# Kernel tuning notes

Hardware: AMD Instinct MI355X
Metric: run time of the kernel (lower is better)

Reference implementation:

```python
import jax, jax.numpy as jnp
import numpy as np

N = 1_000_000
D = 128            # node feature dim
G = 25_000         # number of graphs (num_segments, static)
STEPS = 8


def setup_inputs() -> dict:
    key = jax.random.key(0)
    k1, k2, k3 = jax.random.split(key, 3)
    node_feature = jax.random.normal(k1, (N, D), dtype=jnp.float32)
    graph_indicator = jnp.sort(jax.random.randint(k2, (N,), 0, G, dtype=jnp.int32))
    # glorot-ish small init for recurrent kernel (carry_dim=2D -> 4*D gates)
    recurrent_kernel = jax.random.normal(k3, (2 * D, 4 * D), dtype=jnp.float32) * 0.05
    bias = jnp.zeros((4 * D,), dtype=jnp.float32)
    return {
        "node_feature": node_feature,
        "graph_indicator": graph_indicator,
        "recurrent_kernel": recurrent_kernel,
        "bias": bias,
    }


def _segment_softmax(score, seg_ids, num_segments):
    # numerically-stable per-segment softmax over a flat score vector [N]
    smax = jax.ops.segment_max(score, seg_ids, num_segments=num_segments)
    e = jnp.exp(score - smax[seg_ids])
    denom = jax.ops.segment_sum(e, seg_ids, num_segments=num_segments)
    return e / denom[seg_ids]


def reference(node_feature, graph_indicator, recurrent_kernel, bias):
    d = node_feature.shape[-1]
    memory_state = jnp.zeros((G, d), dtype=node_feature.dtype)
    carry_state = jnp.zeros((G, d), dtype=node_feature.dtype)
    carry_state_evolved = None
    for _ in range(STEPS):
        # attention score per node: <node_feature, carry of its graph>
        carry_exp = carry_state[graph_indicator]                  # [N, d]
        score = jnp.sum(node_feature * carry_exp, axis=1)         # [N]
        attn = _segment_softmax(score, graph_indicator, G)        # [N]
        readout = jax.ops.segment_sum(attn[:, None] * node_feature,
                                      graph_indicator, num_segments=G)  # [G, d]
        carry_state_evolved = jnp.concatenate([carry_state, readout], axis=1)  # [G, 2d]
        # NoInputLSTMCell
        z = carry_state_evolved @ recurrent_kernel + bias          # [G, 4d]
        u, f, c, o = jnp.split(z, 4, axis=1)
        memory_state = jax.nn.sigmoid(f) * memory_state + jax.nn.sigmoid(u) * jnp.tanh(c)
        carry_state = jax.nn.sigmoid(o) * jnp.tanh(memory_state)
    return carry_state_evolved
```

## Files before the change

### kernel.cpp

```cpp
#include <hip/hip_runtime.h>
#include <stdint.h>

#define DD  128
#define G2D 256
#define G4D 512

typedef float  f32x4  __attribute__((ext_vector_type(4)));
typedef short  s16x8  __attribute__((ext_vector_type(8)));
typedef __bf16 bf16x8 __attribute__((ext_vector_type(8)));

__device__ __forceinline__ short f2bf(float f) {
  unsigned u = __builtin_bit_cast(unsigned, f);
  u += 0x7FFFu + ((u >> 16) & 1u);
  return (short)(u >> 16);
}
__device__ __forceinline__ float bf2f(short s) {
  unsigned u = ((unsigned)(unsigned short)s) << 16;
  return __builtin_bit_cast(float, u);
}
__device__ __forceinline__ float sigmoidf_(float x) {
  return 1.f / (1.f + __expf(-x));
}
__device__ __forceinline__ float tanhf_(float x) {
  x = fminf(fmaxf(x, -15.f), 15.f);
  float e = __expf(2.f * x);
  return (e - 1.f) / (e + 1.f);
}

__global__ void seg_kernel(const int* __restrict__ ind, int* __restrict__ seg,
                           int N, int G) {
  int g = blockIdx.x * blockDim.x + threadIdx.x;
  if (g > G) return;
  int lo = 0, hi = N;
  while (lo < hi) {
    int mid = (lo + hi) >> 1;
    if (ind[mid] < g) lo = mid + 1; else hi = mid;
  }
  seg[g] = lo;
}

__global__ void nfconv_kernel(const float* __restrict__ nf,
                              short* __restrict__ nfb) {
  size_t idx = (size_t)blockIdx.x * blockDim.x + threadIdx.x;
  const f32x4* src = (const f32x4*)nf + idx * 2;
  f32x4 a = src[0], b = src[1];
  s16x8 o;
  o[0] = f2bf(a.x); o[1] = f2bf(a.y); o[2] = f2bf(a.z); o[3] = f2bf(a.w);
  o[4] = f2bf(b.x); o[5] = f2bf(b.y); o[6] = f2bf(b.z); o[7] = f2bf(b.w);
  ((s16x8*)nfb)[idx] = o;
}

__global__ void wconv_kernel(const float* __restrict__ W, short* __restrict__ WT) {
  int idx = blockIdx.x * blockDim.x + threadIdx.x;
  int n = idx & (G4D - 1);
  int k = idx >> 9;
  WT[(size_t)n * G2D + k] = f2bf(W[(size_t)k * G4D + n]);
}

__global__ void __launch_bounds__(256) passa_kernel(
    const short* __restrict__ nfb, float* __restrict__ ce,
    const int* __restrict__ seg, int G) {
  int wid = (blockIdx.x * blockDim.x + threadIdx.x) >> 6;
  if (wid >= G) return;
  int lane = threadIdx.x & 63;
  int gq = lane >> 4;
  int sl = lane & 15;
  int s0 = seg[wid], s1 = seg[wid + 1];
  int n  = s1 - s0;
  float* cerow = ce + (size_t)wid * G2D;
  if (n == 0) {
    if (gq == 0) {
      f32x4 z = {0.f, 0.f, 0.f, 0.f};
      *(f32x4*)(cerow + DD + sl * 8)     = z;
      *(f32x4*)(cerow + DD + sl * 8 + 4) = z;
    }
    return;
  }
  f32x4 c0 = *(const f32x4*)(cerow + sl * 8);
  f32x4 c1 = *(const f32x4*)(cerow + sl * 8 + 4);
  float m = -1e30f, l = 0.f;
  float acc[8];
  #pragma unroll
  for (int k = 0; k < 8; k++) acc[k] = 0.f;
  const short* base = nfb + (size_t)s0 * DD + sl * 8;

  auto body = [&](int j) {
    s16x8 xr = *(const s16x8*)(base + (size_t)j * DD);
    float xf[8];
    #pragma unroll
    for (int k = 0; k < 8; k++) xf[k] = bf2f(xr[k]);
    float s = xf[0]*c0.x + xf[1]*c0.y + xf[2]*c0.z + xf[3]*c0.w
            + xf[4]*c1.x + xf[5]*c1.y + xf[6]*c1.z + xf[7]*c1.w;
    #pragma unroll
    for (int off = 1; off < 16; off <<= 1) s += __shfl_xor(s, off, 64);
    float nm = fmaxf(m, s);
    float sc = __expf(m - nm);
    float p  = __expf(s - nm);
    l = l * sc + p;
    #pragma unroll
    for (int k = 0; k < 8; k++) acc[k] = acc[k] * sc + p * xf[k];
    m = nm;
  };

  int nfull = n >> 2;
  #pragma unroll 2
  for (int i = 0; i < nfull; i++) body(i * 4 + gq);
  int rem = n & 3;
  if (gq < rem) body(nfull * 4 + gq);

  #pragma unroll
  for (int w = 16; w <= 32; w <<= 1) {
    float m2 = __shfl_xor(m, w, 64);
    float l2 = __shfl_xor(l, w, 64);
    float M  = fmaxf(m, m2);
    float e1 = __expf(m - M);
    float e2 = __expf(m2 - M);
    l = l * e1 + l2 * e2;
    #pragma unroll
    for (int k = 0; k < 8; k++) {
      float a2 = __shfl_xor(acc[k], w, 64);
      acc[k] = acc[k] * e1 + a2 * e2;
    }
    m = M;
  }
  if (gq == 0) {
    float inv = 1.f / l;
    f32x4 r0, r1;
    r0.x = acc[0]*inv; r0.y = acc[1]*inv; r0.z = acc[2]*inv; r0.w = acc[3]*inv;
    r1.x = acc[4]*inv; r1.y = acc[5]*inv; r1.z = acc[6]*inv; r1.w = acc[7]*inv;
    *(f32x4*)(cerow + DD + sl * 8)     = r0;
    *(f32x4*)(cerow + DD + sl * 8 + 4) = r1;
  }
}

__global__ void __launch_bounds__(256) lstm_kernel(
    float* __restrict__ ce, const short* __restrict__ WT,
    const float* __restrict__ bias, float* __restrict__ mem, int G) {
  __shared__ __align__(16) short As[16][264];
  int m0 = blockIdx.x * 16;
  int t  = threadIdx.x;
  #pragma unroll
  for (int rep = 0; rep < 4; rep++) {
    int idx = rep * 256 + t;
    int row = idx >> 6;
    int cv  = idx & 63;
    int g   = m0 + row;
    f32x4 v = {0.f, 0.f, 0.f, 0.f};
    if (g < G) v = *(const f32x4*)(ce + (size_t)g * G2D + cv * 4);
    As[row][cv * 4 + 0] = f2bf(v.x);
    As[row][cv * 4 + 1] = f2bf(v.y);
    As[row][cv * 4 + 2] = f2bf(v.z);
    As[row][cv * 4 + 3] = f2bf(v.w);
  }
  __syncthreads();
  int wid  = t >> 6;
  int lane = t & 63;
  int quad = lane >> 4;
  int l16  = lane & 15;
  int cb   = wid * 32;
  f32x4 zero4 = {0.f, 0.f, 0.f, 0.f};
  f32x4 acc[4][2];
  #pragma unroll
  for (int gi = 0; gi < 4; gi++)
    #pragma unroll
    for (int ns = 0; ns < 2; ns++) acc[gi][ns] = zero4;
  #pragma unroll
  for (int kc = 0; kc < 8; kc++) {
    int k0 = kc * 32 + quad * 8;
    s16x8 a = *(const s16x8*)(&As[l16][k0]);
    #pragma unroll
    for (int gi = 0; gi < 4; gi++) {
      #pragma unroll
      for (int ns = 0; ns < 2; ns++) {
        int ncol = gi * DD + cb + ns * 16 + l16;
        s16x8 b = *(const s16x8*)(WT + (size_t)ncol * G2D + k0);
        acc[gi][ns] = __builtin_amdgcn_mfma_f32_16x16x32_bf16(
            __builtin_bit_cast(bf16x8, a), __builtin_bit_cast(bf16x8, b),
            acc[gi][ns], 0, 0, 0);
      }
    }
  }
  #pragma unroll
  for (int ns = 0; ns < 2; ns++) {
    int col = cb + ns * 16 + l16;
    float bu = bias[0 * DD + col];
    float bf = bias[1 * DD + col];
    float bc = bias[2 * DD + col];
    float bo = bias[3 * DD + col];
    #pragma unroll
    for (int r = 0; r < 4; r++) {
      int g = m0 + quad * 4 + r;
      if (g < G) {
        float u = acc[0][ns][r] + bu;
        float f = acc[1][ns][r] + bf;
        float c = acc[2][ns][r] + bc;
        float o = acc[3][ns][r] + bo;
        float mo = mem[(size_t)g * DD + col];
        float mn = sigmoidf_(f) * mo + sigmoidf_(u) * tanhf_(c);
        mem[(size_t)g * DD + col] = mn;
        ce[(size_t)g * G2D + col] = sigmoidf_(o) * tanhf_(mn);
      }
    }
  }
}

extern "C" void kernel_launch(void* const* d_in, const int* in_sizes, int n_in,
                              void* d_out, int out_size, void* d_ws, size_t ws_size,
                              hipStream_t stream) {
  const float* nf   = (const float*)d_in[0];
  const int*   ind  = (const int*)d_in[1];
  const float* W    = (const float*)d_in[2];
  const float* bias = (const float*)d_in[3];
  int N = in_sizes[1];
  int G = out_size / G2D;

  char* ws = (char*)d_ws;
  size_t off = 0;
  float* ce  = (float*)(ws + off); off += (size_t)G * G2D * 4;
  float* mem = (float*)(ws + off); off += (size_t)G * DD * 4;
  short* WT  = (short*)(ws + off); off += (size_t)G2D * G4D * 2;
  int*   seg = (int*)(ws + off);   off += (size_t)(G + 1) * 4;
  off = (off + 255) & ~(size_t)255;
  short* nfb = (short*)(ws + off); off += (size_t)N * DD * 2;
  (void)ws_size; (void)n_in;

  nfconv_kernel<<<(int)(((size_t)N * DD / 8 + 255) / 256), 256, 0, stream>>>(nf, nfb);
  hipMemsetAsync(ce, 0, (size_t)G * G2D * 4 + (size_t)G * DD * 4, stream);
  seg_kernel<<<(G + 256) / 256, 256, 0, stream>>>(ind, seg, N, G);
  wconv_kernel<<<(G2D * G4D) / 256, 256, 0, stream>>>(W, WT);

  int pa_blocks   = (G + 3) / 4;
  int lstm_blocks = (G + 15) / 16;
  for (int step = 0; step < 8; step++) {
    passa_kernel<<<pa_blocks, 256, 0, stream>>>(nfb, ce, seg, G);
    if (step < 7)
      lstm_kernel<<<lstm_blocks, 256, 0, stream>>>(ce, WT, bias, mem, G);
  }
  hipMemcpyAsync(d_out, ce, (size_t)out_size * 4, hipMemcpyDeviceToDevice, stream);
}
```

Baseline: 1.587 ms.

## Fuse all attention and LSTM steps into one persistent per-block kernel

Replaces the per-step attention and LSTM kernel launches with a single kernel in which each block owns 16 graphs and iterates all 8 steps. Carry and memory state stay in shared memory instead of round-tripping through global buffers. The bf16 conversion of node features is folded into the first step's pass, and the memset and final copy are removed. The cost is fewer waves per block for the per-graph attention loop (each wave handles 4 graphs sequentially), which may reduce memory-level parallelism on the dominant streaming pass.

```diff
diff --git a/kernel.cpp b/kernel.cpp
--- a/kernel.cpp
+++ b/kernel.cpp
@@ -39,17 +39,6 @@
   seg[g] = lo;
 }
 
-__global__ void nfconv_kernel(const float* __restrict__ nf,
-                              short* __restrict__ nfb) {
-  size_t idx = (size_t)blockIdx.x * blockDim.x + threadIdx.x;
-  const f32x4* src = (const f32x4*)nf + idx * 2;
-  f32x4 a = src[0], b = src[1];
-  s16x8 o;
-  o[0] = f2bf(a.x); o[1] = f2bf(a.y); o[2] = f2bf(a.z); o[3] = f2bf(a.w);
-  o[4] = f2bf(b.x); o[5] = f2bf(b.y); o[6] = f2bf(b.z); o[7] = f2bf(b.w);
-  ((s16x8*)nfb)[idx] = o;
-}
-
 __global__ void wconv_kernel(const float* __restrict__ W, short* __restrict__ WT) {
   int idx = blockIdx.x * blockDim.x + threadIdx.x;
   int n = idx & (G4D - 1);
@@ -57,150 +46,196 @@
   WT[(size_t)n * G2D + k] = f2bf(W[(size_t)k * G4D + n]);
 }
 
-__global__ void __launch_bounds__(256) passa_kernel(
-    const short* __restrict__ nfb, float* __restrict__ ce,
-    const int* __restrict__ seg, int G) {
-  int wid = (blockIdx.x * blockDim.x + threadIdx.x) >> 6;
-  if (wid >= G) return;
-  int lane = threadIdx.x & 63;
-  int gq = lane >> 4;
-  int sl = lane & 15;
-  int s0 = seg[wid], s1 = seg[wid + 1];
-  int n  = s1 - s0;
-  float* cerow = ce + (size_t)wid * G2D;
-  if (n == 0) {
-    if (gq == 0) {
-      f32x4 z = {0.f, 0.f, 0.f, 0.f};
-      *(f32x4*)(cerow + DD + sl * 8)     = z;
-      *(f32x4*)(cerow + DD + sl * 8 + 4) = z;
+__global__ void __launch_bounds__(256) mega_kernel(
+    const float* __restrict__ nf, short* __restrict__ nfb,
+    const int* __restrict__ seg, const short* __restrict__ WT,
+    const float* __restrict__ bias, float* __restrict__ out, int G) {
+  __shared__ __align__(16) short As[16][264];
+  __shared__ float carryS[16][DD];
+  __shared__ float memS[16][DD];
+  const int t  = threadIdx.x;
+  const int m0 = blockIdx.x * 16;
+  #pragma unroll
+  for (int i = 0; i < 8; i++) {
+    int idx = i * 256 + t;
+    ((float*)carryS)[idx] = 0.f;
+    ((float*)memS)[idx]   = 0.f;
+  }
+  const int wid  = t >> 6;
+  const int lane = t & 63;
+  const int gq   = lane >> 4;
+  const int sl   = lane & 15;
+
+  int s0v[4], nv[4];
+  #pragma unroll
+  for (int q = 0; q < 4; q++) {
+    int g = m0 + 4 * wid + q;
+    if (g < G) { s0v[q] = seg[g]; nv[q] = seg[g + 1] - s0v[q]; }
+    else       { s0v[q] = 0;      nv[q] = 0; }
+  }
+  __syncthreads();
+
+  for (int step = 0; step < 8; step++) {
+    const bool last = (step == 7);
+    for (int q = 0; q < 4; q++) {
+      const int row = 4 * wid + q;
+      const int g   = m0 + row;
+      const int n   = nv[q];
+      if (g >= G) continue;
+      if (n == 0) {
+        if (gq == 0) {
+          #pragma unroll
+          for (int k = 0; k < 8; k++) {
+            As[row][DD + sl * 8 + k] = 0;
+            if (last) out[(size_t)g * G2D + DD + sl * 8 + k] = 0.f;
+          }
+        }
+        continue;
+      }
+      float c[8];
+      #pragma unroll
+      for (int k = 0; k < 8; k++) c[k] = carryS[row][sl * 8 + k];
+      float m = -1e30f, l = 0.f;
+      float acc[8];
+      #pragma unroll
+      for (int k = 0; k < 8; k++) acc[k] = 0.f;
+      const int s0 = s0v[q];
+
+      auto accum = [&](const float* xf) {
+        float s = 0.f;
+        #pragma unroll
+        for (int k = 0; k < 8; k++) s += xf[k] * c[k];
+        #pragma unroll
+        for (int off = 1; off < 16; off <<= 1) s += __shfl_xor(s, off, 64);
+        float nm = fmaxf(m, s);
+        float sc = __expf(m - nm);
+        float p  = __expf(s - nm);
+        l = l * sc + p;
+        #pragma unroll
+        for (int k = 0; k < 8; k++) acc[k] = acc[k] * sc + p * xf[k];
+        m = nm;
+      };
+      const int nfull = n >> 2;
+      const int rem   = n & 3;
+      if (step == 0) {
+        const float* basef = nf  + (size_t)s0 * DD + sl * 8;
+        short*       baseb = nfb + (size_t)s0 * DD + sl * 8;
+        auto body0 = [&](int j) {
+          f32x4 a = *(const f32x4*)(basef + (size_t)j * DD);
+          f32x4 b = *(const f32x4*)(basef + (size_t)j * DD + 4);
+          s16x8 xr;
+          xr[0]=f2bf(a.x); xr[1]=f2bf(a.y); xr[2]=f2bf(a.z); xr[3]=f2bf(a.w);
+          xr[4]=f2bf(b.x); xr[5]=f2bf(b.y); xr[6]=f2bf(b.z); xr[7]=f2bf(b.w);
+          *(s16x8*)(baseb + (size_t)j * DD) = xr;
+          float xf[8];
+          #pragma unroll
+          for (int k = 0; k < 8; k++) xf[k] = bf2f(xr[k]);
+          accum(xf);
+        };
+        #pragma unroll 2
+        for (int i = 0; i < nfull; i++) body0(i * 4 + gq);
+        if (gq < rem) body0(nfull * 4 + gq);
+      } else {
+        const short* baseb = nfb + (size_t)s0 * DD + sl * 8;
+        auto body1 = [&](int j) {
+          s16x8 xr = *(const s16x8*)(baseb + (size_t)j * DD);
+          float xf[8];
+          #pragma unroll
+          for (int k = 0; k < 8; k++) xf[k] = bf2f(xr[k]);
+          accum(xf);
+        };
+        #pragma unroll 2
+        for (int i = 0; i < nfull; i++) body1(i * 4 + gq);
+        if (gq < rem) body1(nfull * 4 + gq);
+      }
+      #pragma unroll
+      for (int w = 16; w <= 32; w <<= 1) {
+        float m2 = __shfl_xor(m, w, 64);
+        float l2 = __shfl_xor(l, w, 64);
+        float M  = fmaxf(m, m2);
+        float e1 = __expf(m - M);
+        float e2 = __expf(m2 - M);
+        l = l * e1 + l2 * e2;
+        #pragma unroll
+        for (int k = 0; k < 8; k++) {
+          float a2 = __shfl_xor(acc[k], w, 64);
+          acc[k] = acc[k] * e1 + a2 * e2;
+        }
+        m = M;
+      }
+      if (gq == 0) {
+        float inv = 1.f / l;
+        #pragma unroll
+        for (int k = 0; k < 8; k++) {
+          float r = acc[k] * inv;
+          As[row][DD + sl * 8 + k] = f2bf(r);
+          if (last) out[(size_t)g * G2D + DD + sl * 8 + k] = r;
+        }
+      }
     }
-    return;
-  }
-  f32x4 c0 = *(const f32x4*)(cerow + sl * 8);
-  f32x4 c1 = *(const f32x4*)(cerow + sl * 8 + 4);
-  float m = -1e30f, l = 0.f;
-  float acc[8];
-  #pragma unroll
-  for (int k = 0; k < 8; k++) acc[k] = 0.f;
-  const short* base = nfb + (size_t)s0 * DD + sl * 8;
-
-  auto body = [&](int j) {
-    s16x8 xr = *(const s16x8*)(base + (size_t)j * DD);
-    float xf[8];
-    #pragma unroll
-    for (int k = 0; k < 8; k++) xf[k] = bf2f(xr[k]);
-    float s = xf[0]*c0.x + xf[1]*c0.y + xf[2]*c0.z + xf[3]*c0.w
-            + xf[4]*c1.x + xf[5]*c1.y + xf[6]*c1.z + xf[7]*c1.w;
-    #pragma unroll
-    for (int off = 1; off < 16; off <<= 1) s += __shfl_xor(s, off, 64);
-    float nm = fmaxf(m, s);
-    float sc = __expf(m - nm);
-    float p  = __expf(s - nm);
-    l = l * sc + p;
-    #pragma unroll
-    for (int k = 0; k < 8; k++) acc[k] = acc[k] * sc + p * xf[k];
-    m = nm;
-  };
-
-  int nfull = n >> 2;
-  #pragma unroll 2
-  for (int i = 0; i < nfull; i++) body(i * 4 + gq);
-  int rem = n & 3;
-  if (gq < rem) body(nfull * 4 + gq);
-
-  #pragma unroll
-  for (int w = 16; w <= 32; w <<= 1) {
-    float m2 = __shfl_xor(m, w, 64);
-    float l2 = __shfl_xor(l, w, 64);
-    float M  = fmaxf(m, m2);
-    float e1 = __expf(m - M);
-    float e2 = __expf(m2 - M);
-    l = l * e1 + l2 * e2;
-    #pragma unroll
-    for (int k = 0; k < 8; k++) {
-      float a2 = __shfl_xor(acc[k], w, 64);
-      acc[k] = acc[k] * e1 + a2 * e2;
+    {
+      int row = t >> 4;
+      int c0  = (t & 15) * 8;
+      int g   = m0 + row;
+      if (!last) {
+        #pragma unroll
+        for (int k = 0; k < 8; k++) As[row][c0 + k] = f2bf(carryS[row][c0 + k]);
+      } else if (g < G) {
+        #pragma unroll
+        for (int k = 0; k < 8; k++)
+          out[(size_t)g * G2D + c0 + k] = carryS[row][c0 + k];
+      }
     }
-    m = M;
-  }
-  if (gq == 0) {
-    float inv = 1.f / l;
-    f32x4 r0, r1;
-    r0.x = acc[0]*inv; r0.y = acc[1]*inv; r0.z = acc[2]*inv; r0.w = acc[3]*inv;
-    r1.x = acc[4]*inv; r1.y = acc[5]*inv; r1.z = acc[6]*inv; r1.w = acc[7]*inv;
-    *(f32x4*)(cerow + DD + sl * 8)     = r0;
-    *(f32x4*)(cerow + DD + sl * 8 + 4) = r1;
-  }
-}
-
-__global__ void __launch_bounds__(256) lstm_kernel(
-    float* __restrict__ ce, const short* __restrict__ WT,
-    const float* __restrict__ bias, float* __restrict__ mem, int G) {
-  __shared__ __align__(16) short As[16][264];
-  int m0 = blockIdx.x * 16;
-  int t  = threadIdx.x;
-  #pragma unroll
-  for (int rep = 0; rep < 4; rep++) {
-    int idx = rep * 256 + t;
-    int row = idx >> 6;
-    int cv  = idx & 63;
-    int g   = m0 + row;
-    f32x4 v = {0.f, 0.f, 0.f, 0.f};
-    if (g < G) v = *(const f32x4*)(ce + (size_t)g * G2D + cv * 4);
-    As[row][cv * 4 + 0] = f2bf(v.x);
-    As[row][cv * 4 + 1] = f2bf(v.y);
-    As[row][cv * 4 + 2] = f2bf(v.z);
-    As[row][cv * 4 + 3] = f2bf(v.w);
-  }
-  __syncthreads();
-  int wid  = t >> 6;
-  int lane = t & 63;
-  int quad = lane >> 4;
-  int l16  = lane & 15;
-  int cb   = wid * 32;
-  f32x4 zero4 = {0.f, 0.f, 0.f, 0.f};
-  f32x4 acc[4][2];
-  #pragma unroll
-  for (int gi = 0; gi < 4; gi++)
-    #pragma unroll
-    for (int ns = 0; ns < 2; ns++) acc[gi][ns] = zero4;
-  #pragma unroll
-  for (int kc = 0; kc < 8; kc++) {
-    int k0 = kc * 32 + quad * 8;
-    s16x8 a = *(const s16x8*)(&As[l16][k0]);
-    #pragma unroll
-    for (int gi = 0; gi < 4; gi++) {
+    if (last) break;
+    __syncthreads();
+    {
+      const int cb = wid * 32;
+      f32x4 acc2[4][2];
+      #pragma unroll
+      for (int gi = 0; gi < 4; gi++)
+        #pragma unroll
+        for (int ns = 0; ns < 2; ns++) { f32x4 z = {0.f,0.f,0.f,0.f}; acc2[gi][ns] = z; }
+      #pragma unroll
+      for (int kc = 0; kc < 8; kc++) {
+        int k0 = kc * 32 + gq * 8;
+        s16x8 a = *(const s16x8*)(&As[sl][k0]);
+        #pragma unroll
+        for (int gi = 0; gi < 4; gi++) {
+          #pragma unroll
+          for (int ns = 0; ns < 2; ns++) {
+            int ncol = gi * DD + cb + ns * 16 + sl;
+            s16x8 b = *(const s16x8*)(WT + (size_t)ncol * G2D + k0);
+            acc2[gi][ns] = __builtin_amdgcn_mfma_f32_16x16x32_bf16(
+                __builtin_bit_cast(bf16x8, a), __builtin_bit_cast(bf16x8, b),
+                acc2[gi][ns], 0, 0, 0);
+          }
+        }
+      }
       #pragma unroll
       for (int ns = 0; ns < 2; ns++) {
-        int ncol = gi * DD + cb + ns * 16 + l16;
-        s16x8 b = *(const s16x8*)(WT + (size_t)ncol * G2D + k0);
-        acc[gi][ns] = __builtin_amdgcn_mfma_f32_16x16x32_bf16(
-            __builtin_bit_cast(bf16x8, a), __builtin_bit_cast(bf16x8, b),
-            acc[gi][ns], 0, 0, 0);
+        int col = cb + ns * 16 + sl;
+        float bu = bias[0 * DD + col];
+        float bf = bias[1 * DD + col];
+        float bc = bias[2 * DD + col];
+        float bo = bias[3 * DD + col];
+        #pragma unroll
+        for (int r = 0; r < 4; r++) {
+          int row = gq * 4 + r;
+          int g   = m0 + row;
+          if (g < G) {
+            float u = acc2[0][ns][r] + bu;
+            float f = acc2[1][ns][r] + bf;
+            float c = acc2[2][ns][r] + bc;
+            float o = acc2[3][ns][r] + bo;
+            float mo = memS[row][col];
+            float mn = sigmoidf_(f) * mo + sigmoidf_(u) * tanhf_(c);
+            memS[row][col]   = mn;
+            carryS[row][col] = sigmoidf_(o) * tanhf_(mn);
+          }
+        }
       }
     }
-  }
-  #pragma unroll
-  for (int ns = 0; ns < 2; ns++) {
-    int col = cb + ns * 16 + l16;
-    float bu = bias[0 * DD + col];
-    float bf = bias[1 * DD + col];
-    float bc = bias[2 * DD + col];
-    float bo = bias[3 * DD + col];
-    #pragma unroll
-    for (int r = 0; r < 4; r++) {
-      int g = m0 + quad * 4 + r;
-      if (g < G) {
-        float u = acc[0][ns][r] + bu;
-        float f = acc[1][ns][r] + bf;
-        float c = acc[2][ns][r] + bc;
-        float o = acc[3][ns][r] + bo;
-        float mo = mem[(size_t)g * DD + col];
-        float mn = sigmoidf_(f) * mo + sigmoidf_(u) * tanhf_(c);
-        mem[(size_t)g * DD + col] = mn;
-        ce[(size_t)g * G2D + col] = sigmoidf_(o) * tanhf_(mn);
-      }
-    }
+    __syncthreads();
   }
 }
 
@@ -216,25 +251,13 @@
 
   char* ws = (char*)d_ws;
   size_t off = 0;
-  float* ce  = (float*)(ws + off); off += (size_t)G * G2D * 4;
-  float* mem = (float*)(ws + off); off += (size_t)G * DD * 4;
+  short* nfb = (short*)(ws + off); off += (size_t)N * DD * 2;
   short* WT  = (short*)(ws + off); off += (size_t)G2D * G4D * 2;
   int*   seg = (int*)(ws + off);   off += (size_t)(G + 1) * 4;
-  off = (off + 255) & ~(size_t)255;
-  short* nfb = (short*)(ws + off); off += (size_t)N * DD * 2;
   (void)ws_size; (void)n_in;
 
-  nfconv_kernel<<<(int)(((size_t)N * DD / 8 + 255) / 256), 256, 0, stream>>>(nf, nfb);
-  hipMemsetAsync(ce, 0, (size_t)G * G2D * 4 + (size_t)G * DD * 4, stream);
   seg_kernel<<<(G + 256) / 256, 256, 0, stream>>>(ind, seg, N, G);
   wconv_kernel<<<(G2D * G4D) / 256, 256, 0, stream>>>(W, WT);
-
-  int pa_blocks   = (G + 3) / 4;
-  int lstm_blocks = (G + 15) / 16;
-  for (int step = 0; step < 8; step++) {
-    passa_kernel<<<pa_blocks, 256, 0, stream>>>(nfb, ce, seg, G);
-    if (step < 7)
-      lstm_kernel<<<lstm_blocks, 256, 0, stream>>>(ce, WT, bias, mem, G);
-  }
-  hipMemcpyAsync(d_out, ce, (size_t)out_size * 4, hipMemcpyDeviceToDevice, stream);
-}
+  mega_kernel<<<(G + 15) / 16, 256, 0, stream>>>(nf, nfb, seg, WT, bias,
+                                                 (float*)d_out, G);
+}
```

New measurement: 2.157 ms. 35.9% more time.
